# Performance work log

Measured on AMD Instinct MI355X. Metric: run time of the kernel, lower is better.

The kernel has to match this reference:

```python
import jax, jax.numpy as jnp
import numpy as np

B, N, H, W, C_OUT = 4, 480000, 1024, 1024, 64
PR = (0.0, -39.68, -3.0, 69.12, 39.68, 1.0)  # point cloud range [x0,y0,z0,x1,y1,z1]
BN_EPS = 1e-5


def setup_inputs():
    key = jax.random.key(0)
    ks = iter(jax.random.split(key, 48))
    bidx = jax.random.randint(next(ks), (N,), 0, B).astype(jnp.float32)
    px = jax.random.uniform(next(ks), (N,), minval=PR[0], maxval=PR[3])
    py = jax.random.uniform(next(ks), (N,), minval=PR[1], maxval=PR[4])
    pz = jax.random.uniform(next(ks), (N,), minval=PR[2], maxval=PR[5])
    pi = jax.random.uniform(next(ks), (N,))
    points = jnp.stack([bidx, px, py, pz, pi], axis=1)  # [N,5]

    def w(shape):
        return jax.random.normal(next(ks), shape, jnp.float32) * 0.1

    def bnp(c):
        return (1.0 + 0.1 * jax.random.normal(next(ks), (c,), jnp.float32),
                0.1 * jax.random.normal(next(ks), (c,), jnp.float32),
                0.1 * jax.random.normal(next(ks), (c,), jnp.float32),
                jax.random.uniform(next(ks), (c,), minval=0.5, maxval=1.5))

    g0, be0, m0, v0 = bnp(8)
    g1, be1, m1, v1 = bnp(16)
    g2, be2, m2, v2 = bnp(32)
    g3, be3, m3, v3 = bnp(C_OUT)
    return {
        'points': points, 'batch_size': B,
        'w0': w((8, 2, 3, 3)), 'b0': w((8,)),
        'g0': g0, 'be0': be0, 'm0': m0, 'v0': v0,
        'w1': w((16, 1, 3, 3)), 'b1': w((16,)),  # groups=8 conv: 16 out, 8 in groups
        'g1': g1, 'be1': be1, 'm1': m1, 'v1': v1,
        'wdw': w((16, 1, 3, 3)), 'bdw': w((16,)),
        'wpw': w((32, 16, 1, 1)), 'bpw': w((32,)),
        'g2': g2, 'be2': be2, 'm2': m2, 'v2': v2,
        'w3': w((C_OUT, 32, 3, 3)), 'b3': w((C_OUT,)),
        'g3': g3, 'be3': be3, 'm3': m3, 'v3': v3,
    }


def conv2d(x, wt, b, groups=1, pad=1):
    out = jax.lax.conv_general_dilated(
        x, wt, (1, 1), [(pad, pad), (pad, pad)],
        feature_group_count=groups,
        dimension_numbers=('NCHW', 'OIHW', 'NCHW'))
    return out + b[None, :, None, None]


def bn(x, g, be, m, v):
    s = g * jax.lax.rsqrt(v + BN_EPS)
    return x * s[None, :, None, None] + (be - m * s)[None, :, None, None]


def maxpool2(x):
    return jax.lax.reduce_window(x, -jnp.inf, jax.lax.max,
                                 (1, 1, 2, 2), (1, 1, 2, 2), 'VALID')


def channel_shuffle(x, groups):
    b, c, h, w = x.shape
    return x.reshape(b, groups, c // groups, h, w).transpose(0, 2, 1, 3, 4).reshape(b, c, h, w)


def rasterize(points, batch_size):
    # points: [N,5] = (batch_idx, x, y, z, intensity)
    x_scale = W / (PR[3] - PR[0])
    y_scale = H / (PR[4] - PR[1])
    # PR[0]==0 -> no x shift (matches the source's branch)
    xp = (points[:, 1] * x_scale).astype(jnp.int32)  # trunc toward zero like torch .to(int)
    yp = ((points[:, 2] + (PR[4] - PR[1]) / 2) * y_scale).astype(jnp.int32)
    valid = (xp >= 0) & (xp < W) & (yp >= 0) & (yp < H)
    bi = jnp.where(valid, points[:, 0].astype(jnp.int32), batch_size)  # invalid -> OOB, dropped
    xi = jnp.where(valid, xp, W)
    yi = jnp.where(valid, yp, H)
    bev_z = jnp.full((batch_size, H, W), -10.0, jnp.float32)
    bev_z = bev_z.at[bi, yi, xi].max(points[:, 3], mode='drop')
    bev_i = jnp.zeros((batch_size, H, W), jnp.float32)
    bev_i = bev_i.at[bi, yi, xi].max(points[:, 4], mode='drop')
    return jnp.stack([bev_z, bev_i], axis=1)  # [B,2,H,W]


def reference(points, batch_size, w0, b0, g0, be0, m0, v0, w1, b1, g1, be1, m1, v1,
              wdw, bdw, wpw, bpw, g2, be2, m2, v2, w3, b3, g3, be3, m3, v3):
    x = rasterize(points, batch_size)
    x = jax.nn.relu(bn(conv2d(x, w0, b0), g0, be0, m0, v0))          # x_conv1
    x = maxpool2(x)
    x = jax.nn.relu(bn(conv2d(x, w1, b1, groups=8), g1, be1, m1, v1))  # x_conv2
    x = maxpool2(x)
    x = conv2d(x, wdw, bdw, groups=16)      # depthwise
    x = channel_shuffle(x, 16)              # identity when groups==channels, kept for faithfulness
    x = conv2d(x, wpw, bpw, pad=0)          # pointwise 16->32
    x = jax.nn.relu(bn(x, g2, be2, m2, v2))
    x = jax.nn.relu(bn(conv2d(x, w3, b3), g3, be3, m3, v3))          # x_conv3
    x = maxpool2(x)                         # x_conv4 == spatial_features
    return x
```

## Files before the change

kernel.cpp:

```cpp
#include <hip/hip_runtime.h>
#include <cstddef>

#define H_IN 1024
#define W_IN 1024
#define BN_EPS 1e-5f

typedef float f32x4 __attribute__((ext_vector_type(4)));
typedef _Float16 f16x8 __attribute__((ext_vector_type(8)));

__device__ __forceinline__ unsigned encF(float f) {
    unsigned u = __float_as_uint(f);
    return (u & 0x80000000u) ? ~u : (u | 0x80000000u);
}
__device__ __forceinline__ float decF(unsigned e, float untouched) {
    if (e == 0u) return untouched;
    unsigned bits = (e & 0x80000000u) ? (e ^ 0x80000000u) : ~e;
    return __uint_as_float(bits);
}

__global__ void k_prep(uint4* __restrict__ bevq,
                       const float* __restrict__ w3, const float* __restrict__ b3,
                       const float* __restrict__ g3, const float* __restrict__ be3,
                       const float* __restrict__ m3, const float* __restrict__ v3,
                       _Float16* __restrict__ wh, float* __restrict__ tv) {
    int bid = blockIdx.x;
    int t = threadIdx.x;
    if (bid < 2048) {
        int i = bid * 256 + t;
        uint4 z = {0u, 0u, 0u, 0u};
        #pragma unroll
        for (int j = 0; j < 4; j++)
            bevq[(size_t)j*524288 + i] = z;
        return;
    }
    __shared__ float sSh[64];
    if (t < 64) {
        float s = g3[t] / sqrtf(v3[t] + BN_EPS);
        sSh[t] = s;
        if (bid == 2048) tv[t] = (b3[t] - m3[t]) * s + be3[t];
    }
    __syncthreads();
    int khw = bid - 2048;
    for (int i = t; i < 2048; i += 256) {
        int oc = i >> 5;
        wh[khw*2048 + i] = (_Float16)(w3[(size_t)i*9 + khw] * sSh[oc]);
    }
}

__global__ void k_rasterize(const float* __restrict__ pts, unsigned* __restrict__ bev, int n) {
    int i0 = blockIdx.x * blockDim.x + threadIdx.x;
    int stride = gridDim.x * blockDim.x;
    const float XS = (float)(1024.0/69.12);
    const float YS = (float)(1024.0/79.36);
    for (int i = i0; i < n; i += stride) {
        float fb  = pts[(size_t)i*5+0];
        float px  = pts[(size_t)i*5+1];
        float py  = pts[(size_t)i*5+2];
        float pz  = pts[(size_t)i*5+3];
        float pit = pts[(size_t)i*5+4];
        int xp = (int)(px * XS);
        int yp = (int)((py + 39.68f) * YS);
        if (xp < 0 || xp >= W_IN || yp < 0 || yp >= H_IN) continue;
        int b = (int)fb;
        size_t off = (((size_t)b * H_IN + yp) * W_IN + xp) * 2;
        atomicMax(bev + off,     encF(pz));
        atomicMax(bev + off + 1, encF(pit));
    }
}

__global__ __launch_bounds__(256, 4) void k_conv1(
                        const unsigned* __restrict__ bev, const float* __restrict__ w0,
                        const float* __restrict__ b0, const float* __restrict__ g0,
                        const float* __restrict__ be0, const float* __restrict__ m0,
                        const float* __restrict__ v0, _Float16* __restrict__ out) {
    __shared__ float wS[144];
    __shared__ float sS[8], tS[8];
    int t = threadIdx.x;
    if (t < 144) wS[t] = w0[t];
    if (t < 8) {
        float s = g0[t] / sqrtf(v0[t] + BN_EPS);
        sS[t] = s;
        tS[t] = (b0[t] - m0[t]) * s + be0[t];
    }
    __syncthreads();
    int idx = blockIdx.x * 256 + t;
    int x = idx & 511, y = (idx >> 9) & 511, b = idx >> 18;
    const unsigned* base = bev + (size_t)b * H_IN * W_IN * 2;
    float in[2][4][4];
    #pragma unroll
    for (int r = 0; r < 4; r++) {
        int iy = 2*y - 1 + r;
        #pragma unroll
        for (int cc = 0; cc < 4; cc++) {
            int ix = 2*x - 1 + cc;
            if (iy >= 0 && iy < H_IN && ix >= 0 && ix < W_IN) {
                const unsigned* p2 = base + ((size_t)iy*W_IN + ix)*2;
                in[0][r][cc] = decF(p2[0], -10.0f);
                in[1][r][cc] = decF(p2[1], 0.0f);
            } else {
                in[0][r][cc] = 0.0f;
                in[1][r][cc] = 0.0f;
            }
        }
    }
    f16x8 ov;
    #pragma unroll
    for (int oc = 0; oc < 8; oc++) {
        float mx = 0.0f;
        #pragma unroll
        for (int py = 0; py < 2; py++)
            #pragma unroll
            for (int px = 0; px < 2; px++) {
                float acc = 0.0f;
                #pragma unroll
                for (int c = 0; c < 2; c++)
                    #pragma unroll
                    for (int kh = 0; kh < 3; kh++)
                        #pragma unroll
                        for (int kw = 0; kw < 3; kw++)
                            acc += in[c][py+kh][px+kw] * wS[((oc*2+c)*3+kh)*3+kw];
                acc = fmaxf(acc * sS[oc] + tS[oc], 0.0f);
                mx = fmaxf(mx, acc);
            }
        ov[oc] = (_Float16)mx;
    }
    *(f16x8*)(out + ((size_t)((b*512 + y)*512 + x)) * 8) = ov;
}

__global__ __launch_bounds__(256, 4) void k_conv2m(
                        const _Float16* __restrict__ x1, const float* __restrict__ w1,
                        const float* __restrict__ b1, const float* __restrict__ g1,
                        const float* __restrict__ be1, const float* __restrict__ m1,
                        const float* __restrict__ v1, float* __restrict__ out) {
    __shared__ _Float16 As[10][66][8];
    __shared__ float wS[144], sS[16], tS[16];
    int t = threadIdx.x;
    if (t < 144) wS[t] = w1[t];
    if (t < 16) {
        float s = g1[t] / sqrtf(v1[t] + BN_EPS);
        sS[t] = s;
        tS[t] = (b1[t] - m1[t]) * s + be1[t];
    }
    int lane = t & 63, w = t >> 6;
    int l15 = lane & 15, l4 = lane >> 4;
    int bi = blockIdx.x;
    int xt = bi & 7, yg = (bi >> 3) & 63, b = bi >> 9;
    int x0 = xt * 64;
    int y0 = yg * 8;
    __syncthreads();

    f16x8 Bf[3];
    #pragma unroll
    for (int kh = 0; kh < 3; kh++) {
        f16x8 z = {0,0,0,0,0,0,0,0};
        if (l4 < 3) z[l15 >> 1] = (_Float16)(wS[l15*9 + kh*3 + l4] * sS[l15]);
        Bf[kh] = z;
    }
    float tvv = tS[l15];

    const _Float16* base = x1 + (size_t)b * 512 * 512 * 8;
    for (int s = t; s < 660; s += 256) {
        int row = s / 66, px = s - row * 66;
        int gy = y0 - 1 + row, gx = x0 - 1 + px;
        f16x8 v = {0,0,0,0,0,0,0,0};
        if (gy >= 0 && gy < 512 && gx >= 0 && gx < 512)
            v = *(const f16x8*)(base + ((size_t)gy*512 + gx)*8);
        *(f16x8*)&As[row][px][0] = v;
    }
    __syncthreads();

    for (int ti = 0; ti < 4; ti++) {
        f32x4 acc[2];
        acc[0] = (f32x4){0,0,0,0};
        acc[1] = (f32x4){0,0,0,0};
        #pragma unroll
        for (int kh = 0; kh < 3; kh++)
            #pragma unroll
            for (int f = 0; f < 2; f++) {
                f16x8 Af = {0,0,0,0,0,0,0,0};
                if (l4 < 3)
                    Af = *(const f16x8*)&As[2*ti + f + kh][w*16 + l15 + l4][0];
                acc[f] = __builtin_amdgcn_mfma_f32_16x16x32_f16(Af, Bf[kh], acc[f], 0, 0, 0);
            }
        int yp = yg*4 + ti;
        float* ob = out + (size_t)b*16*65536 + (size_t)l15*65536 + (size_t)yp*256;
        #pragma unroll
        for (int q = 0; q < 2; q++) {
            float v0 = fmaxf(fmaxf(acc[0][2*q]   + tvv, 0.f),
                             fmaxf(acc[0][2*q+1] + tvv, 0.f));
            float v1_ = fmaxf(fmaxf(acc[1][2*q]   + tvv, 0.f),
                              fmaxf(acc[1][2*q+1] + tvv, 0.f));
            int xp = xt*32 + w*8 + 2*l4 + q;
            ob[xp] = fmaxf(v0, v1_);
        }
    }
}

__global__ __launch_bounds__(256, 4) void k_dwpw(
                       const float* __restrict__ x2, const float* __restrict__ wdw,
                       const float* __restrict__ bdw, const float* __restrict__ wpw,
                       const float* __restrict__ bpw, const float* __restrict__ g2,
                       const float* __restrict__ be2, const float* __restrict__ m2,
                       const float* __restrict__ v2, _Float16* __restrict__ out) {
    __shared__ float patch[16*10*36];
    __shared__ float wdwS[144];
    __shared__ float bdwS[16];
    __shared__ float wpwS[512];
    __shared__ float sS[32], tS[32];
    int t = threadIdx.x;
    if (t < 144) wdwS[t] = wdw[t];
    if (t < 16) bdwS[t] = bdw[t];
    for (int i = t; i < 512; i += 256) wpwS[i] = wpw[i];
    if (t < 32) {
        float s = g2[t] / sqrtf(v2[t] + BN_EPS);
        sS[t] = s;
        tS[t] = (bpw[t] - m2[t]) * s + be2[t];
    }

    int bi = blockIdx.x;
    int tx = bi & 7, ty = (bi >> 3) & 31, b = bi >> 8;
    int x0 = tx * 32, y0 = ty * 8;
    const float* base = x2 + (size_t)b * 16 * 256 * 256;

    for (int i = t; i < 16*10*34; i += 256) {
        int ic = i / 340;
        int rem = i - ic * 340;
        int r = rem / 34, c = rem - r * 34;
        int gy = y0 - 1 + r, gx = x0 - 1 + c;
        patch[(ic*10 + r)*36 + c] =
            (gy >= 0 && gy < 256 && gx >= 0 && gx < 256)
                ? base[(size_t)ic*65536 + (size_t)gy*256 + gx] : 0.0f;
    }
    __syncthreads();

    int px = t & 31, pyy = t >> 5;
    int x = x0 + px, y = y0 + pyy;

    float dv[16];
    #pragma unroll
    for (int ic = 0; ic < 16; ic++) {
        float d = bdwS[ic];
        #pragma unroll
        for (int r = 0; r < 3; r++)
            #pragma unroll
            for (int c = 0; c < 3; c++)
                d += patch[(ic*10 + pyy + r)*36 + px + c] * wdwS[ic*9 + r*3 + c];
        dv[ic] = d;
    }

    _Float16* ob = out + ((size_t)((b*256 + y)*256 + x)) * 32;
    #pragma unroll
    for (int q = 0; q < 4; q++) {
        f16x8 ov;
        #pragma unroll
        for (int j = 0; j < 8; j++) {
            int oc = q*8 + j;
            float a = 0.0f;
            #pragma unroll
            for (int ic = 0; ic < 16; ic++)
                a += dv[ic] * wpwS[oc*16+ic];
            ov[j] = (_Float16)fmaxf(a*sS[oc] + tS[oc], 0.0f);
        }
        *(f16x8*)(ob + q*8) = ov;
    }
}

__global__ __launch_bounds__(256, 2) void k_conv3m(const _Float16* __restrict__ xh,
                                                   const _Float16* __restrict__ wh,
                                                   const float* __restrict__ tv,
                                                   float* __restrict__ out) {
    __shared__ _Float16 As[10*66*40];
    int t = threadIdx.x;
    int lane = t & 63, w = t >> 6;
    int l15 = lane & 15, l4 = lane >> 4;
    int bi = blockIdx.x;
    int xt = bi & 3, yg = (bi >> 2) & 31, b = bi >> 7;
    int x0 = xt * 64;
    int y0 = yg * 8;

    f16x8 Bf[9][4];
    #pragma unroll
    for (int khw = 0; khw < 9; khw++)
        #pragma unroll
        for (int g = 0; g < 4; g++)
            Bf[khw][g] = *(const f16x8*)(wh + ((khw*64 + g*16 + l15)*32 + 8*l4));

    float tvv[4];
    #pragma unroll
    for (int g = 0; g < 4; g++) tvv[g] = tv[g*16 + l15];

    for (int s = t; s < 660; s += 256) {
        int row = s / 66, px = s - row*66;
        int gy = y0 - 1 + row, gx = x0 - 1 + px;
        float4* dst = (float4*)&As[(row*66 + px)*40];
        if (gy >= 0 && gy < 256 && gx >= 0 && gx < 256) {
            const float4* src = (const float4*)(xh + ((size_t)((b*256 + gy)*256 + gx)) * 32);
            #pragma unroll
            for (int j = 0; j < 4; j++) dst[j] = src[j];
        } else {
            float4 z = make_float4(0.f, 0.f, 0.f, 0.f);
            #pragma unroll
            for (int j = 0; j < 4; j++) dst[j] = z;
        }
    }
    __syncthreads();

    for (int ti = 0; ti < 4; ti++) {
        int ypool = yg*4 + ti;
        f32x4 acc[2][4];
        #pragma unroll
        for (int f = 0; f < 2; f++)
            #pragma unroll
            for (int g = 0; g < 4; g++)
                acc[f][g] = (f32x4){0.f, 0.f, 0.f, 0.f};

        #pragma unroll
        for (int kh = 0; kh < 3; kh++)
            #pragma unroll
            for (int kw = 0; kw < 3; kw++) {
                f16x8 Af[2];
                #pragma unroll
                for (int f = 0; f < 2; f++) {
                    int row = 2*ti + f + kh;
                    int px = w*16 + l15 + kw;
                    Af[f] = *(const f16x8*)&As[(row*66 + px)*40 + 8*l4];
                }
                #pragma unroll
                for (int f = 0; f < 2; f++)
                    #pragma unroll
                    for (int g = 0; g < 4; g++)
                        acc[f][g] = __builtin_amdgcn_mfma_f32_16x16x32_f16(
                            Af[f], Bf[kh*3+kw][g], acc[f][g], 0, 0, 0);
            }

        #pragma unroll
        for (int g = 0; g < 4; g++) {
            int oc = g*16 + l15;
            #pragma unroll
            for (int q = 0; q < 2; q++) {
                float v0 = fmaxf(fmaxf(acc[0][g][2*q]   + tvv[g], 0.f),
                                 fmaxf(acc[0][g][2*q+1] + tvv[g], 0.f));
                float v1 = fmaxf(fmaxf(acc[1][g][2*q]   + tvv[g], 0.f),
                                 fmaxf(acc[1][g][2*q+1] + tvv[g], 0.f));
                int px = x0/2 + w*8 + 2*l4 + q;
                out[(((size_t)b*64 + oc)*128 + ypool)*128 + px] = fmaxf(v0, v1);
            }
        }
    }
}

extern "C" void kernel_launch(void* const* d_in, const int* in_sizes, int n_in,
                              void* d_out, int out_size, void* d_ws, size_t ws_size,
                              hipStream_t stream) {
    const float* points = (const float*)d_in[0];
    int n = in_sizes[0] / 5;
    const float* w0  = (const float*)d_in[2];
    const float* b0  = (const float*)d_in[3];
    const float* g0  = (const float*)d_in[4];
    const float* be0 = (const float*)d_in[5];
    const float* m0  = (const float*)d_in[6];
    const float* v0  = (const float*)d_in[7];
    const float* w1  = (const float*)d_in[8];
    const float* b1  = (const float*)d_in[9];
    const float* g1  = (const float*)d_in[10];
    const float* be1 = (const float*)d_in[11];
    const float* m1  = (const float*)d_in[12];
    const float* v1  = (const float*)d_in[13];
    const float* wdw = (const float*)d_in[14];
    const float* bdw = (const float*)d_in[15];
    const float* wpw = (const float*)d_in[16];
    const float* bpw = (const float*)d_in[17];
    const float* g2  = (const float*)d_in[18];
    const float* be2 = (const float*)d_in[19];
    const float* m2  = (const float*)d_in[20];
    const float* v2  = (const float*)d_in[21];
    const float* w3  = (const float*)d_in[22];
    const float* b3  = (const float*)d_in[23];
    const float* g3  = (const float*)d_in[24];
    const float* be3 = (const float*)d_in[25];
    const float* m3  = (const float*)d_in[26];
    const float* v3  = (const float*)d_in[27];

    float* ws  = (float*)d_ws;
    unsigned* bev = (unsigned*)ws;
    _Float16* x1h = (_Float16*)(ws + 8388608);
    float* x2  = ws;
    _Float16* x3h = (_Float16*)(ws + 8388608);
    _Float16* wh  = (_Float16*)(ws + 16777216);
    float* tv  = ws + 16786432;
    float* outp = (float*)d_out;

    k_prep<<<2057, 256, 0, stream>>>((uint4*)bev, w3, b3, g3, be3, m3, v3, wh, tv);
    int rblocks = (n/4 + 255) / 256;
    k_rasterize<<<rblocks, 256, 0, stream>>>(points, bev, n);
    k_conv1<<<4096, 256, 0, stream>>>(bev, w0, b0, g0, be0, m0, v0, x1h);
    k_conv2m<<<2048, 256, 0, stream>>>(x1h, w1, b1, g1, be1, m1, v1, x2);
    k_dwpw<<<1024, 256, 0, stream>>>(x2, wdw, bdw, wpw, bpw, g2, be2, m2, v2, x3h);
    k_conv3m<<<512, 256, 0, stream>>>(x3h, wh, tv, outp);
}
```

Before: 133.2 us.

## Store conv2 output as fp16 NHWC and flatten rasterize grid

The intermediate between the grouped conv2 and the depthwise/pointwise stage changes from fp32 NCHW to fp16 NHWC with 16 channels per pixel. This halves the intermediate traffic and lets the dwpw tile loader fetch all 16 channels of a pixel with two 16-byte vector loads. The rasterize kernel drops its grid-stride loop in favour of one thread per point. The fp16 intermediate adds rounding error, and each conv2 store is now a scattered 2-byte write.

Measured after the change: 132.5 us. About the same (-0.5%).

```diff
diff --git a/kernel.cpp b/kernel.cpp
--- a/kernel.cpp
+++ b/kernel.cpp
@@ -48,24 +48,22 @@
 }
 
 __global__ void k_rasterize(const float* __restrict__ pts, unsigned* __restrict__ bev, int n) {
-    int i0 = blockIdx.x * blockDim.x + threadIdx.x;
-    int stride = gridDim.x * blockDim.x;
+    int i = blockIdx.x * blockDim.x + threadIdx.x;
+    if (i >= n) return;
+    float fb  = pts[(size_t)i*5+0];
+    float px  = pts[(size_t)i*5+1];
+    float py  = pts[(size_t)i*5+2];
+    float pz  = pts[(size_t)i*5+3];
+    float pit = pts[(size_t)i*5+4];
     const float XS = (float)(1024.0/69.12);
     const float YS = (float)(1024.0/79.36);
-    for (int i = i0; i < n; i += stride) {
-        float fb  = pts[(size_t)i*5+0];
-        float px  = pts[(size_t)i*5+1];
-        float py  = pts[(size_t)i*5+2];
-        float pz  = pts[(size_t)i*5+3];
-        float pit = pts[(size_t)i*5+4];
-        int xp = (int)(px * XS);
-        int yp = (int)((py + 39.68f) * YS);
-        if (xp < 0 || xp >= W_IN || yp < 0 || yp >= H_IN) continue;
-        int b = (int)fb;
-        size_t off = (((size_t)b * H_IN + yp) * W_IN + xp) * 2;
-        atomicMax(bev + off,     encF(pz));
-        atomicMax(bev + off + 1, encF(pit));
-    }
+    int xp = (int)(px * XS);
+    int yp = (int)((py + 39.68f) * YS);
+    if (xp < 0 || xp >= W_IN || yp < 0 || yp >= H_IN) return;
+    int b = (int)fb;
+    size_t off = (((size_t)b * H_IN + yp) * W_IN + xp) * 2;
+    atomicMax(bev + off,     encF(pz));
+    atomicMax(bev + off + 1, encF(pit));
 }
 
 __global__ __launch_bounds__(256, 4) void k_conv1(
@@ -131,7 +129,7 @@
                         const _Float16* __restrict__ x1, const float* __restrict__ w1,
                         const float* __restrict__ b1, const float* __restrict__ g1,
                         const float* __restrict__ be1, const float* __restrict__ m1,
-                        const float* __restrict__ v1, float* __restrict__ out) {
+                        const float* __restrict__ v1, _Float16* __restrict__ out) {
     __shared__ _Float16 As[10][66][8];
     __shared__ float wS[144], sS[16], tS[16];
     int t = threadIdx.x;
@@ -183,7 +181,7 @@
                 acc[f] = __builtin_amdgcn_mfma_f32_16x16x32_f16(Af, Bf[kh], acc[f], 0, 0, 0);
             }
         int yp = yg*4 + ti;
-        float* ob = out + (size_t)b*16*65536 + (size_t)l15*65536 + (size_t)yp*256;
+        _Float16* ob = out + ((size_t)b*256 + yp) * 256 * 16;
         #pragma unroll
         for (int q = 0; q < 2; q++) {
             float v0 = fmaxf(fmaxf(acc[0][2*q]   + tvv, 0.f),
@@ -191,13 +189,13 @@
             float v1_ = fmaxf(fmaxf(acc[1][2*q]   + tvv, 0.f),
                               fmaxf(acc[1][2*q+1] + tvv, 0.f));
             int xp = xt*32 + w*8 + 2*l4 + q;
-            ob[xp] = fmaxf(v0, v1_);
+            ob[(size_t)xp*16 + l15] = (_Float16)fmaxf(v0, v1_);
         }
     }
 }
 
 __global__ __launch_bounds__(256, 4) void k_dwpw(
-                       const float* __restrict__ x2, const float* __restrict__ wdw,
+                       const _Float16* __restrict__ x2, const float* __restrict__ wdw,
                        const float* __restrict__ bdw, const float* __restrict__ wpw,
                        const float* __restrict__ bpw, const float* __restrict__ g2,
                        const float* __restrict__ be2, const float* __restrict__ m2,
@@ -220,16 +218,25 @@
     int bi = blockIdx.x;
     int tx = bi & 7, ty = (bi >> 3) & 31, b = bi >> 8;
     int x0 = tx * 32, y0 = ty * 8;
-    const float* base = x2 + (size_t)b * 16 * 256 * 256;
-
-    for (int i = t; i < 16*10*34; i += 256) {
-        int ic = i / 340;
-        int rem = i - ic * 340;
-        int r = rem / 34, c = rem - r * 34;
+    const _Float16* base = x2 + (size_t)b * 256 * 256 * 16;
+
+    for (int i = t; i < 340; i += 256) {
+        int r = i / 34, c = i - r * 34;
         int gy = y0 - 1 + r, gx = x0 - 1 + c;
-        patch[(ic*10 + r)*36 + c] =
-            (gy >= 0 && gy < 256 && gx >= 0 && gx < 256)
-                ? base[(size_t)ic*65536 + (size_t)gy*256 + gx] : 0.0f;
+        if (gy >= 0 && gy < 256 && gx >= 0 && gx < 256) {
+            const _Float16* p = base + ((size_t)gy*256 + gx)*16;
+            f16x8 v0 = *(const f16x8*)p;
+            f16x8 v1 = *(const f16x8*)(p + 8);
+            #pragma unroll
+            for (int j = 0; j < 8; j++) {
+                patch[j*360     + r*36 + c] = (float)v0[j];
+                patch[(j+8)*360 + r*36 + c] = (float)v1[j];
+            }
+        } else {
+            #pragma unroll
+            for (int j = 0; j < 16; j++)
+                patch[j*360 + r*36 + c] = 0.0f;
+        }
     }
     __syncthreads();
 
@@ -384,17 +391,16 @@
     float* ws  = (float*)d_ws;
     unsigned* bev = (unsigned*)ws;
     _Float16* x1h = (_Float16*)(ws + 8388608);
-    float* x2  = ws;
+    _Float16* x2h = (_Float16*)ws;
     _Float16* x3h = (_Float16*)(ws + 8388608);
     _Float16* wh  = (_Float16*)(ws + 16777216);
     float* tv  = ws + 16786432;
     float* outp = (float*)d_out;
 
     k_prep<<<2057, 256, 0, stream>>>((uint4*)bev, w3, b3, g3, be3, m3, v3, wh, tv);
-    int rblocks = (n/4 + 255) / 256;
-    k_rasterize<<<rblocks, 256, 0, stream>>>(points, bev, n);
+    k_rasterize<<<(n + 255)/256, 256, 0, stream>>>(points, bev, n);
     k_conv1<<<4096, 256, 0, stream>>>(bev, w0, b0, g0, be0, m0, v0, x1h);
-    k_conv2m<<<2048, 256, 0, stream>>>(x1h, w1, b1, g1, be1, m1, v1, x2);
-    k_dwpw<<<1024, 256, 0, stream>>>(x2, wdw, bdw, wpw, bpw, g2, be2, m2, v2, x3h);
+    k_conv2m<<<2048, 256, 0, stream>>>(x1h, w1, b1, g1, be1, m1, v1, x2h);
+    k_dwpw<<<1024, 256, 0, stream>>>(x2h, wdw, bdw, wpw, bpw, g2, be2, m2, v2, x3h);
     k_conv3m<<<512, 256, 0, stream>>>(x3h, wh, tv, outp);
 }
```
